# Kernel optimization log

Measured on AMD Instinct MI355X. Metric: run time of the kernel, lower is better.

The kernel has to match this reference:

```python
import jax, jax.numpy as jnp
import numpy as np

OUT_FEATURES = 4096
IN_FEATURES = 4096
GROUP_SIZE = 128
N_GROUPS = OUT_FEATURES * IN_FEATURES // GROUP_SIZE  # 131072


def setup_inputs() -> dict:
    key = jax.random.key(0)
    k_x, k_t, k_s = jax.random.split(key, 3)
    x = jax.random.normal(k_x, (4, 2048, IN_FEATURES), dtype=jnp.float32)
    # ternary codes in {-1, 0, 1}, stored as int (int8 in the original module)
    ternary = jax.random.randint(k_t, (OUT_FEATURES, IN_FEATURES), 0, 3, dtype=jnp.int32) - 1
    # per-group positive scales (beta = mean |w| per group in the original init)
    scales = jax.random.uniform(k_s, (N_GROUPS,), dtype=jnp.float32, minval=0.01, maxval=0.1)
    return {"x": x, "ternary": ternary, "scales": scales}


def reference(x, ternary, scales):
    # Dequantize: expand per-group scale across group_size, multiply ternary sign.
    w = (ternary.astype(jnp.float32).reshape(-1, GROUP_SIZE) * scales[:, None])
    w = w.reshape(OUT_FEATURES, IN_FEATURES)
    # F.linear(x, W) = x @ W.T
    return jnp.einsum('bsi,oi->bso', x, w)
```

## Files before the change

kernel.cpp:

```cpp
#include <hip/hip_runtime.h>
#include <hip/hip_bf16.h>


#define Msz 8192
#define Nsz 4096
#define Ksz 4096

typedef __attribute__((ext_vector_type(8))) short short8;
typedef __attribute__((ext_vector_type(4))) float f32x4;
typedef __attribute__((ext_vector_type(4))) int int4v;
typedef __attribute__((ext_vector_type(4))) float float4v;
typedef __attribute__((ext_vector_type(8))) unsigned short ushort8;

static __device__ __forceinline__ unsigned short f2bf(float f) {
    unsigned u = __builtin_bit_cast(unsigned, f);
    u += 0x7fffu + ((u >> 16) & 1u);
    return (unsigned short)(u >> 16);
}

__global__ void prep(const float* __restrict__ x, const int* __restrict__ t,
                     const float* __restrict__ s,
                     unsigned short* __restrict__ ox, unsigned short* __restrict__ ow) {
    if (blockIdx.x < 2048) {
        int i = blockIdx.x * 256 + threadIdx.x;
        for (; i < Msz * Ksz / 8; i += 2048 * 256) {
            const float4v* p = (const float4v*)x + (size_t)i * 2;
            float4v a = p[0], b = p[1];
            ushort8 r;
            r[0] = f2bf(a[0]); r[1] = f2bf(a[1]); r[2] = f2bf(a[2]); r[3] = f2bf(a[3]);
            r[4] = f2bf(b[0]); r[5] = f2bf(b[1]); r[6] = f2bf(b[2]); r[7] = f2bf(b[3]);
            *((ushort8*)ox + i) = r;
        }
    } else {
        int i = (blockIdx.x - 2048) * 256 + threadIdx.x;
        for (; i < Nsz * Ksz / 8; i += 1024 * 256) {
            float sc = s[i >> 4];
            const int4v* p = (const int4v*)t + (size_t)i * 2;
            int4v a = p[0], b = p[1];
            ushort8 r;
            r[0] = f2bf((float)a[0] * sc); r[1] = f2bf((float)a[1] * sc);
            r[2] = f2bf((float)a[2] * sc); r[3] = f2bf((float)a[3] * sc);
            r[4] = f2bf((float)b[0] * sc); r[5] = f2bf((float)b[1] * sc);
            r[6] = f2bf((float)b[2] * sc); r[7] = f2bf((float)b[3] * sc);
            *((ushort8*)ow + i) = r;
        }
    }
}


#define READ_B(b) {                                                              \
    _Pragma("unroll") for (int n = 0; n < 4; ++n)                                \
    _Pragma("unroll") for (int ks = 0; ks < 2; ++ks)                             \
      bfr[n][ks] = *(const short8*)(L + (b)*65536 + 32768 + ((((wc)*4+n)*2+ks)<<10) + laneA); }

#define READ_A(b, q) {                                                           \
    _Pragma("unroll") for (int m = 0; m < 2; ++m)                                \
    _Pragma("unroll") for (int ks = 0; ks < 2; ++ks)                             \
      af[m][ks] = *(const short8*)(L + (b)*65536 + ((((q)*4+(wr)*2+m)*2+ks)<<10) + laneA); }

#define MFMAS(q) {                                                               \
    _Pragma("unroll") for (int m = 0; m < 2; ++m)                                \
    _Pragma("unroll") for (int n = 0; n < 4; ++n) {                              \
      acc[(q)*2+m][n] = __builtin_amdgcn_mfma_f32_16x16x32_bf16(af[m][0], bfr[n][0], acc[(q)*2+m][n], 0, 0, 0); \
      acc[(q)*2+m][n] = __builtin_amdgcn_mfma_f32_16x16x32_bf16(af[m][1], bfr[n][1], acc[(q)*2+m][n], 0, 0, 0); } }

#define STAGE_H(PM, MOFF, BOFF, T, H) {                                          \
    _Pragma("unroll") for (int j = 0; j < 2; ++j)                                \
      __builtin_amdgcn_global_load_lds(                                          \
        (const __attribute__((address_space(1))) void*)(PM + (size_t)((H)*128 + j*64)*Ksz + (T)*64), \
        (__attribute__((address_space(3))) void*)(L + (BOFF) + (MOFF) + (H)*16384 + j*8192 + dOff), \
        16, 0, 0); }

#define WAITV6 asm volatile("s_waitcnt vmcnt(6)" ::: "memory");

#define PHASE(READS, QM, STG, WV)                                                \
    READS;                                                                       \
    STG;                                                                         \
    __builtin_amdgcn_sched_barrier(0);                                           \
    __builtin_amdgcn_s_barrier();                                                \
    asm volatile("s_waitcnt lgkmcnt(0)" ::: "memory");                           \
    __builtin_amdgcn_sched_barrier(0);                                           \
    __builtin_amdgcn_s_setprio(1);                                               \
    MFMAS(QM);                                                                   \
    __builtin_amdgcn_s_setprio(0);                                               \
    WV;                                                                          \
    __builtin_amdgcn_sched_barrier(0);                                           \
    __builtin_amdgcn_s_barrier();                                                \
    __builtin_amdgcn_sched_barrier(0);

__global__ __launch_bounds__(512, 2) void gemm_8p(const unsigned short* __restrict__ A,
                                                  const unsigned short* __restrict__ B,
                                                  float* __restrict__ C) {
    __shared__ __align__(16) unsigned char L[131072];

    const int tid  = threadIdx.x;
    const int lane = tid & 63;
    const int wid  = tid >> 6;
    const int wr   = wid >> 2;
    const int wc   = wid & 3;
    const int rowBase = blockIdx.y * 256;
    const int colBase = blockIdx.x * 256;

    const int laneA = (((lane & 15) * 64) + ((lane >> 4) * 16)) ^ (((lane >> 3) & 1) << 5);
    const int kloc = (lane & 1) * 8 + (((lane >> 1) ^ (lane >> 5)) & 1) * 16;
    const int r_st = lane >> 2;
    const int dOff = wid * 1024;

    const unsigned short* pAb = A + (size_t)(rowBase + (wid >> 1) * 16 + r_st) * Ksz + (wid & 1) * 32 + kloc;
    const unsigned short* pBb = B + (size_t)(colBase + (wid >> 1) * 16 + r_st) * Ksz + (wid & 1) * 32 + kloc;

    f32x4 acc[8][4] = {};
    short8 af[2][2], bfr[4][2];

    STAGE_H(pBb, 32768, 0,     0, 0);
    STAGE_H(pAb, 0,     0,     0, 0);
    STAGE_H(pBb, 32768, 0,     0, 1);
    STAGE_H(pAb, 0,     0,     0, 1);
    STAGE_H(pBb, 32768, 65536, 1, 0);
    STAGE_H(pAb, 0,     65536, 1, 1);
    STAGE_H(pBb, 32768, 65536, 1, 1);
    WAITV6
    __builtin_amdgcn_sched_barrier(0);
    __builtin_amdgcn_s_barrier();
    __builtin_amdgcn_sched_barrier(0);

    for (int i = 0; i < 32; ++i) {
        const int t1 = 2 * i + 1;
        const int t2 = (i < 31) ? 2 * i + 2 : 62;
        const int t3 = (i < 31) ? 2 * i + 3 : 62;

        PHASE({ READ_B(0); READ_A(0, 0); }, 0, STAGE_H(pAb, 0,     65536, t1, 0), )
        PHASE(READ_A(0, 1),                 1, STAGE_H(pBb, 32768, 0,     t2, 0), )
        PHASE(READ_A(0, 2),                 2, STAGE_H(pAb, 0,     0,     t2, 0), )
        PHASE(READ_A(0, 3),                 3, STAGE_H(pBb, 32768, 0,     t2, 1), WAITV6)
        PHASE({ READ_B(1); READ_A(1, 2); }, 2, STAGE_H(pAb, 0,     0,     t2, 1), )
        PHASE(READ_A(1, 3),                 3, STAGE_H(pBb, 32768, 65536, t3, 0), )
        PHASE(READ_A(1, 0),                 0, STAGE_H(pAb, 0,     65536, t3, 1), )
        PHASE(READ_A(1, 1),                 1, STAGE_H(pBb, 32768, 65536, t3, 1), WAITV6)
    }

    asm volatile("s_waitcnt vmcnt(0)" ::: "memory");

    const int crl = (lane >> 4) * 4;
    const int ccol0 = colBase + wc * 64 + (lane & 15);
#pragma unroll
    for (int q = 0; q < 4; ++q)
#pragma unroll
        for (int m = 0; m < 2; ++m)
#pragma unroll
            for (int n = 0; n < 4; ++n) {
                const int row0 = rowBase + (q * 4 + wr * 2 + m) * 16 + crl;
                float* cp = C + (size_t)row0 * Nsz + ccol0 + n * 16;
#pragma unroll
                for (int j = 0; j < 4; ++j)
                    cp[(size_t)j * Nsz] = acc[q * 2 + m][n][j];
            }
}

__global__ void gemm_naive(const float* __restrict__ x, const int* __restrict__ t,
                           const float* __restrict__ s, float* __restrict__ C) {
    size_t o = (size_t)blockIdx.x * blockDim.x + threadIdx.x;
    if (o >= (size_t)Msz * Nsz) return;
    int m = (int)(o / Nsz), n = (int)(o % Nsz);
    float acc = 0.f;
    for (int g = 0; g < Ksz / 128; ++g) {
        float sc = s[n * (Ksz / 128) + g];
        float p = 0.f;
        const float* xp = x + (size_t)m * Ksz + g * 128;
        const int* tp = t + (size_t)n * Ksz + g * 128;
        for (int k = 0; k < 128; ++k) p += xp[k] * (float)tp[k];
        acc += sc * p;
    }
    C[o] = acc;
}

extern "C" void kernel_launch(void* const* d_in, const int* in_sizes, int n_in,
                              void* d_out, int out_size, void* d_ws, size_t ws_size,
                              hipStream_t stream) {
    const float* x      = (const float*)d_in[0];
    const int*   tern   = (const int*)d_in[1];
    const float* scales = (const float*)d_in[2];
    float* out = (float*)d_out;

    const size_t aBytes = (size_t)Msz * Ksz * 2;
    const size_t bBytes = (size_t)Nsz * Ksz * 2;

    if (ws_size >= aBytes + bBytes) {
        unsigned short* Abf = (unsigned short*)d_ws;
        unsigned short* Bbf = (unsigned short*)((char*)d_ws + aBytes);
        prep<<<3072, 256, 0, stream>>>(x, tern, scales, Abf, Bbf);
        dim3 grid(Nsz / 256, Msz / 256);
        gemm_8p<<<grid, 512, 0, stream>>>(Abf, Bbf, out);
    } else {
        gemm_naive<<<(int)(((size_t)Msz * Nsz + 255) / 256), 256, 0, stream>>>(x, tern, scales, out);
    }
}
```

Baseline: 266.8 us.

## Restructure GEMM main loop into two-barrier sections with double A fragments

Replaces the eight single-quarter phases per iteration (each with two barriers) with two sections per buffer, each doing two quarters of MFMAs between barriers. Two sets of A fragment registers allow the LDS reads for two quarters to be issued together. Global-to-LDS staging is reordered so the B tiles and the A tile for the next buffer are issued after the first barrier. The intent is fewer barriers and waitcnt stalls per K step, at the cost of more registers and a riskier buffer-reuse ordering.

```diff
diff --git a/kernel.cpp b/kernel.cpp
--- a/kernel.cpp
+++ b/kernel.cpp
@@ -48,21 +48,21 @@
 }
 
 
-#define READ_B(b) {                                                              \
+#define READ_Bv(b) {                                                             \
     _Pragma("unroll") for (int n = 0; n < 4; ++n)                                \
     _Pragma("unroll") for (int ks = 0; ks < 2; ++ks)                             \
       bfr[n][ks] = *(const short8*)(L + (b)*65536 + 32768 + ((((wc)*4+n)*2+ks)<<10) + laneA); }
 
-#define READ_A(b, q) {                                                           \
+#define READ_Aq(S, b, q) {                                                       \
     _Pragma("unroll") for (int m = 0; m < 2; ++m)                                \
     _Pragma("unroll") for (int ks = 0; ks < 2; ++ks)                             \
-      af[m][ks] = *(const short8*)(L + (b)*65536 + ((((q)*4+(wr)*2+m)*2+ks)<<10) + laneA); }
-
-#define MFMAS(q) {                                                               \
+      S[m][ks] = *(const short8*)(L + (b)*65536 + ((((q)*4+(wr)*2+m)*2+ks)<<10) + laneA); }
+
+#define MFMAS_Q(q, AF) {                                                         \
     _Pragma("unroll") for (int m = 0; m < 2; ++m)                                \
     _Pragma("unroll") for (int n = 0; n < 4; ++n) {                              \
-      acc[(q)*2+m][n] = __builtin_amdgcn_mfma_f32_16x16x32_bf16(af[m][0], bfr[n][0], acc[(q)*2+m][n], 0, 0, 0); \
-      acc[(q)*2+m][n] = __builtin_amdgcn_mfma_f32_16x16x32_bf16(af[m][1], bfr[n][1], acc[(q)*2+m][n], 0, 0, 0); } }
+      acc[(q)*2+m][n] = __builtin_amdgcn_mfma_f32_16x16x32_bf16(AF[m][0], bfr[n][0], acc[(q)*2+m][n], 0, 0, 0); \
+      acc[(q)*2+m][n] = __builtin_amdgcn_mfma_f32_16x16x32_bf16(AF[m][1], bfr[n][1], acc[(q)*2+m][n], 0, 0, 0); } }
 
 #define STAGE_H(PM, MOFF, BOFF, T, H) {                                          \
     _Pragma("unroll") for (int j = 0; j < 2; ++j)                                \
@@ -71,22 +71,37 @@
         (__attribute__((address_space(3))) void*)(L + (BOFF) + (MOFF) + (H)*16384 + j*8192 + dOff), \
         16, 0, 0); }
 
-#define WAITV6 asm volatile("s_waitcnt vmcnt(6)" ::: "memory");
-
-#define PHASE(READS, QM, STG, WV)                                                \
-    READS;                                                                       \
-    STG;                                                                         \
+#define BAR_ONLY                                                                 \
     __builtin_amdgcn_sched_barrier(0);                                           \
     __builtin_amdgcn_s_barrier();                                                \
-    asm volatile("s_waitcnt lgkmcnt(0)" ::: "memory");                           \
+    __builtin_amdgcn_sched_barrier(0);
+
+#define BAR_V6                                                                   \
     __builtin_amdgcn_sched_barrier(0);                                           \
+    asm volatile("s_waitcnt vmcnt(6)" ::: "memory");                             \
+    __builtin_amdgcn_s_barrier();                                                \
+    __builtin_amdgcn_sched_barrier(0);
+
+#define SECTION(b, TA1, TBA)                                                     \
+    STAGE_H(pAb, 0, (1-(b))*65536, TA1, 1);                                      \
+    READ_Bv(b);                                                                  \
+    READ_Aq(afA, b, 0);                                                          \
+    READ_Aq(afB, b, 1);                                                          \
     __builtin_amdgcn_s_setprio(1);                                               \
-    MFMAS(QM);                                                                   \
+    MFMAS_Q(0, afA);                                                             \
+    MFMAS_Q(1, afB);                                                             \
     __builtin_amdgcn_s_setprio(0);                                               \
-    WV;                                                                          \
-    __builtin_amdgcn_sched_barrier(0);                                           \
-    __builtin_amdgcn_s_barrier();                                                \
-    __builtin_amdgcn_sched_barrier(0);
+    BAR_ONLY                                                                     \
+    STAGE_H(pBb, 32768, (b)*65536, TBA, 0);                                      \
+    STAGE_H(pBb, 32768, (b)*65536, TBA, 1);                                      \
+    STAGE_H(pAb, 0,     (b)*65536, TBA, 0);                                      \
+    READ_Aq(afA, b, 2);                                                          \
+    READ_Aq(afB, b, 3);                                                          \
+    __builtin_amdgcn_s_setprio(1);                                               \
+    MFMAS_Q(2, afA);                                                             \
+    MFMAS_Q(3, afB);                                                             \
+    __builtin_amdgcn_s_setprio(0);                                               \
+    BAR_V6
 
 __global__ __launch_bounds__(512, 2) void gemm_8p(const unsigned short* __restrict__ A,
                                                   const unsigned short* __restrict__ B,
@@ -110,17 +125,18 @@
     const unsigned short* pBb = B + (size_t)(colBase + (wid >> 1) * 16 + r_st) * Ksz + (wid & 1) * 32 + kloc;
 
     f32x4 acc[8][4] = {};
-    short8 af[2][2], bfr[4][2];
+    short8 afA[2][2], afB[2][2], bfr[4][2];
 
     STAGE_H(pBb, 32768, 0,     0, 0);
+    STAGE_H(pBb, 32768, 0,     0, 1);
     STAGE_H(pAb, 0,     0,     0, 0);
-    STAGE_H(pBb, 32768, 0,     0, 1);
     STAGE_H(pAb, 0,     0,     0, 1);
     STAGE_H(pBb, 32768, 65536, 1, 0);
+    STAGE_H(pBb, 32768, 65536, 1, 1);
+    STAGE_H(pAb, 0,     65536, 1, 0);
     STAGE_H(pAb, 0,     65536, 1, 1);
-    STAGE_H(pBb, 32768, 65536, 1, 1);
-    WAITV6
-    __builtin_amdgcn_sched_barrier(0);
+    __builtin_amdgcn_sched_barrier(0);
+    asm volatile("s_waitcnt vmcnt(8)" ::: "memory");
     __builtin_amdgcn_s_barrier();
     __builtin_amdgcn_sched_barrier(0);
 
@@ -129,17 +145,11 @@
         const int t2 = (i < 31) ? 2 * i + 2 : 62;
         const int t3 = (i < 31) ? 2 * i + 3 : 62;
 
-        PHASE({ READ_B(0); READ_A(0, 0); }, 0, STAGE_H(pAb, 0,     65536, t1, 0), )
-        PHASE(READ_A(0, 1),                 1, STAGE_H(pBb, 32768, 0,     t2, 0), )
-        PHASE(READ_A(0, 2),                 2, STAGE_H(pAb, 0,     0,     t2, 0), )
-        PHASE(READ_A(0, 3),                 3, STAGE_H(pBb, 32768, 0,     t2, 1), WAITV6)
-        PHASE({ READ_B(1); READ_A(1, 2); }, 2, STAGE_H(pAb, 0,     0,     t2, 1), )
-        PHASE(READ_A(1, 3),                 3, STAGE_H(pBb, 32768, 65536, t3, 0), )
-        PHASE(READ_A(1, 0),                 0, STAGE_H(pAb, 0,     65536, t3, 1), )
-        PHASE(READ_A(1, 1),                 1, STAGE_H(pBb, 32768, 65536, t3, 1), WAITV6)
-    }
-
-    asm volatile("s_waitcnt vmcnt(0)" ::: "memory");
+        SECTION(0, t1, t2)
+        SECTION(1, t2, t3)
+    }
+
+    asm volatile("s_waitcnt vmcnt(0) lgkmcnt(0)" ::: "memory");
 
     const int crl = (lane >> 4) * 4;
     const int ccol0 = colBase + wc * 64 + (lane & 15);
```

After: 266.6 us. No clear change (-0.1%).
